# Kernel optimization log

Hardware: AMD Instinct MI355X
Metric: run time of the kernel (lower is better)

## Reference

```python
import jax, jax.numpy as jnp
import numpy as np

N, D_FEAT, HIDDEN, HEADS, NUM_CLASSES = 6000, 512, 256, 8, 32
NEG_INF = -1e9
LEAKY_ALPHA = 0.2


def gat_head(x, adj_bias, W, a1, a2):
    """Single dense GAT attention head (NSL GraphAttnLayer, inference mode).

    x: [N, D], W: [D, F], a1/a2: [F]. Returns [N, F].
    """
    h = x @ W                       # [N, F]
    f1 = h @ a1                     # [N] source term
    f2 = h @ a2                     # [N] destination term
    e = jax.nn.leaky_relu(f1[:, None] + f2[None, :], LEAKY_ALPHA) + adj_bias
    coefs = jax.nn.softmax(e, axis=-1)  # softmax over neighbors j
    return coefs @ h                # [N, F]


def setup_inputs() -> dict:
    key = jax.random.key(0)
    ks = jax.random.split(key, 8)
    features = jax.random.normal(ks[0], (N, D_FEAT), dtype=jnp.float32)
    adj = jax.random.randint(ks[1], (N, N), 0, 2, dtype=jnp.int32)
    # Block 0: 8 heads, each D_FEAT -> HIDDEN
    W0 = jax.random.normal(ks[2], (HEADS, D_FEAT, HIDDEN), dtype=jnp.float32) / np.sqrt(D_FEAT)
    a10 = jax.random.normal(ks[3], (HEADS, HIDDEN), dtype=jnp.float32) / np.sqrt(HIDDEN)
    a20 = jax.random.normal(ks[4], (HEADS, HIDDEN), dtype=jnp.float32) / np.sqrt(HIDDEN)
    # Classifier: single head, HEADS*HIDDEN -> NUM_CLASSES
    Wc = jax.random.normal(ks[5], (HEADS * HIDDEN, NUM_CLASSES), dtype=jnp.float32) / np.sqrt(HEADS * HIDDEN)
    a1c = jax.random.normal(ks[6], (NUM_CLASSES,), dtype=jnp.float32) / np.sqrt(NUM_CLASSES)
    a2c = jax.random.normal(ks[7], (NUM_CLASSES,), dtype=jnp.float32) / np.sqrt(NUM_CLASSES)
    return {"features": features, "adj": adj, "W0": W0, "a10": a10,
            "a20": a20, "Wc": Wc, "a1c": a1c, "a2c": a2c}


def reference(features, adj, W0, a10, a20, Wc, a1c, a2c):
    adj_bias = jnp.where(adj > 0, 0.0, NEG_INF).astype(jnp.float32)  # [N, N]
    # GATBlock: 8 heads concatenated, then ELU (dropout is identity at inference)
    heads = [gat_head(features, adj_bias, W0[h], a10[h], a20[h]) for h in range(HEADS)]
    x = jax.nn.elu(jnp.concatenate(heads, axis=1))  # [N, HEADS*HIDDEN]
    # Classifier GraphAttnLayer -> [N, NUM_CLASSES]
    return gat_head(x, adj_bias, Wc, a1c, a2c)
```

## Files before the change

### kernel.cpp

```cpp
#include <hip/hip_runtime.h>
#include <hip/hip_bf16.h>

#define NN 6000
#define NPAD 6016
#define DF 512
#define HID 256
#define NH 8
#define NC 32
#define FTOT 2048
#define MSTR 96
#define NJB (NPAD / 64)
#define L2E 1.4426950408889634f

using short8 = __attribute__((ext_vector_type(8))) short;
using f32x16 = __attribute__((ext_vector_type(16))) float;
using f32x4  = __attribute__((ext_vector_type(4))) float;

__device__ __forceinline__ unsigned short f2bf(float f) {
    unsigned int u = __float_as_uint(f);
    return (unsigned short)((u + 0x7fffu + ((u >> 16) & 1u)) >> 16);
}
__device__ __forceinline__ float bf2f(unsigned short s) {
    return __uint_as_float(((unsigned int)s) << 16);
}
__device__ __forceinline__ void gl16(const void* g, void* l) {
    __builtin_amdgcn_global_load_lds(
        (const __attribute__((address_space(1))) unsigned int*)g,
        (__attribute__((address_space(3))) unsigned int*)l, 16, 0, 0);
}


__global__ void pack_bits(const int* __restrict__ adj, unsigned char* __restrict__ maskb) {
    int row = blockIdx.y;
    int b = blockIdx.x * 256 + threadIdx.x;
    if (b >= 768) return;
    int j0 = b * 8;
    unsigned int v = 0;
    if (j0 + 7 < NN) {
        const int4* p = (const int4*)(adj + (size_t)row * NN + j0);
        int4 a = p[0], c = p[1];
        v = (unsigned)((a.x>0) | ((a.y>0)<<1) | ((a.z>0)<<2) | ((a.w>0)<<3)
          | ((c.x>0)<<4) | ((c.y>0)<<5) | ((c.z>0)<<6) | ((c.w>0)<<7));
    }
    maskb[(size_t)row * 768 + b] = (unsigned char)v;
}

__global__ void cast_x4(const float* __restrict__ x, unsigned short* __restrict__ xb, int n4) {
    int i = blockIdx.x * 256 + threadIdx.x;
    if (i >= n4) return;
    float4 v = ((const float4*)x)[i];
    unsigned long long pk = (unsigned long long)f2bf(v.x)
        | ((unsigned long long)f2bf(v.y) << 16)
        | ((unsigned long long)f2bf(v.z) << 32)
        | ((unsigned long long)f2bf(v.w) << 48);
    ((unsigned long long*)xb)[i] = pk;
}

__global__ void wt_pack(const float* __restrict__ W0, unsigned short* __restrict__ Wt) {
    int fp = blockIdx.x;
    int h = fp >> 8, f = fp & 255;
    for (int k = threadIdx.x; k < DF; k += 256)
        Wt[(size_t)fp * DF + k] = f2bf(W0[(((size_t)h * DF + k) << 8) | f]);
}

__global__ void wct_pack(const float* __restrict__ Wc, unsigned short* __restrict__ Wct) {
    int c = blockIdx.x;
    for (int k = threadIdx.x; k < FTOT; k += 256)
        Wct[(size_t)c * FTOT + k] = f2bf(Wc[(size_t)k * NC + c]);
}

__global__ __launch_bounds__(256, 2) void gemm_h(const unsigned short* __restrict__ A,
                                                 const unsigned short* __restrict__ B,
                                                 unsigned short* __restrict__ Ht) {
    __shared__ __align__(16) unsigned short As[128 * 64];
    __shared__ __align__(16) unsigned short Bs[128 * 64];
    const int w = threadIdx.x >> 6, l = threadIdx.x & 63;
    const int lrow = l & 31, kh = l >> 5;
    const int wm = w >> 1, wn = w & 1;
    const int mbase = blockIdx.x * 128, nbase = blockIdx.y * 128;
    const int srcc = (l & 7) ^ (l >> 3);
    f32x16 acc[2][2];
#pragma unroll
    for (int i = 0; i < 2; ++i)
#pragma unroll
        for (int j = 0; j < 2; ++j) acc[i][j] = (f32x16)0.0f;

#pragma unroll 1
    for (int kb = 0; kb < DF / 64; ++kb) {
        __syncthreads();
#pragma unroll
        for (int q = 0; q < 4; ++q) {
            int c = q * 4 + w;
            int r = c * 8 + (l >> 3);
            int arow = mbase + r; if (arow > NN - 1) arow = NN - 1;
            gl16(A + (size_t)arow * DF + kb * 64 + srcc * 8, (char*)As + c * 1024);
            gl16(B + (size_t)(nbase + r) * DF + kb * 64 + srcc * 8, (char*)Bs + c * 1024);
        }
        __syncthreads();
#pragma unroll
        for (int kk = 0; kk < 4; ++kk) {
            short8 av[2], bv[2];
#pragma unroll
            for (int mt = 0; mt < 2; ++mt) {
                int r = wm * 64 + mt * 32 + lrow;
                av[mt] = *(const short8*)((const char*)As + r * 128 + ((((kk << 1) | kh) ^ (r & 7)) << 4));
            }
#pragma unroll
            for (int ft = 0; ft < 2; ++ft) {
                int r = wn * 64 + ft * 32 + lrow;
                bv[ft] = *(const short8*)((const char*)Bs + r * 128 + ((((kk << 1) | kh) ^ (r & 7)) << 4));
            }
#pragma unroll
            for (int mt = 0; mt < 2; ++mt)
#pragma unroll
                for (int ft = 0; ft < 2; ++ft)
                    acc[mt][ft] = __builtin_amdgcn_mfma_f32_32x32x16_bf16(av[mt], bv[ft], acc[mt][ft], 0, 0, 0);
        }
    }
#pragma unroll
    for (int mt = 0; mt < 2; ++mt)
#pragma unroll
        for (int ft = 0; ft < 2; ++ft) {
            size_t n = nbase + wn * 64 + ft * 32 + lrow;
#pragma unroll
            for (int g = 0; g < 4; ++g) {
                int m0 = mbase + wm * 64 + mt * 32 + (g << 3) + (kh << 2);
                unsigned long long pk =
                    (unsigned long long)f2bf(acc[mt][ft][g * 4 + 0]) |
                    ((unsigned long long)f2bf(acc[mt][ft][g * 4 + 1]) << 16) |
                    ((unsigned long long)f2bf(acc[mt][ft][g * 4 + 2]) << 32) |
                    ((unsigned long long)f2bf(acc[mt][ft][g * 4 + 3]) << 48);
                *(unsigned long long*)(Ht + n * NPAD + m0) = pk;
            }
        }
}

__global__ void f12_kern(const unsigned short* __restrict__ Ht, const float* __restrict__ a1,
                         const float* __restrict__ a2, float* __restrict__ f1, float* __restrict__ f2,
                         int fdim) {
    int h = blockIdx.y;
    int i = blockIdx.x * 256 + threadIdx.x;
    if (i >= NPAD) return;
    float s1 = 0.f, s2 = 0.f;
    const unsigned short* base = Ht + (size_t)h * fdim * NPAD + i;
    for (int f = 0; f < fdim; ++f) {
        float v = bf2f(base[(size_t)f * NPAD]);
        s1 = fmaf(v, a1[h * fdim + f], s1);
        s2 = fmaf(v, a2[h * fdim + f], s2);
    }
    f1[(size_t)h * NPAD + i] = s1 * L2E;
    f2[(size_t)h * NPAD + i] = s2 * L2E;
}

__global__ void rarb_kern(const float* __restrict__ f1all, const float* __restrict__ f2all,
                          float* __restrict__ RA, float* __restrict__ RB,
                          float* __restrict__ E2F, float* __restrict__ E2Fb) {
    int h = blockIdx.x;
    __shared__ float red[8];
    const float* f2h = f2all + (size_t)h * NPAD;
    float m = -3.0e38f;
    for (int i = threadIdx.x; i < NN; i += 256) m = fmaxf(m, f2h[i]);
    for (int off = 32; off; off >>= 1) m = fmaxf(m, __shfl_xor(m, off));
    if ((threadIdx.x & 63) == 0) red[threadIdx.x >> 6] = m;
    __syncthreads();
    if (threadIdx.x == 0)
        red[4] = fmaxf(fmaxf(red[0], red[1]), fmaxf(red[2], red[3]));
    __syncthreads();
    float Mh = red[4];
    for (int i = threadIdx.x; i < NPAD; i += 256) {
        float F1 = (i < NN) ? f1all[(size_t)h * NPAD + i] : 0.f;
        float t2 = F1 + Mh;
        float Mi = fmaxf(t2, 0.2f * t2);
        RA[(size_t)h * NPAD + i] = F1 - Mi;
        RB[(size_t)h * NPAD + i] = 0.2f * F1 - Mi;
        float v2 = f2h[i];
        E2F[(size_t)h * NPAD + i] = exp2f(v2);
        E2Fb[(size_t)h * NPAD + i] = exp2f(0.2f * v2);
    }
}

__global__ __launch_bounds__(256, 3) void attn_main(
    const unsigned short* __restrict__ Ht,
    const unsigned long long* __restrict__ mask,
    const float* __restrict__ RA, const float* __restrict__ RB,
    const float* __restrict__ E2F, const float* __restrict__ E2Fb,
    unsigned short* __restrict__ x2)
{
    __shared__ __align__(16) unsigned short htile[3 * 128 * 64];
    const int bid = blockIdx.x;
    const int h = bid & 7;
    const int fh = (bid >> 3) & 1;
    const int rowbase = (bid >> 4) * 128;
    const int w = threadIdx.x >> 6, l = threadIdx.x & 63;
    const int lrow = l & 31, kh = l >> 5;
    const int myrow = rowbase + w * 32 + lrow;
    const bool act = myrow < NN;
    const int rowc = act ? myrow : NN - 1;
    const unsigned short* Hh = Ht + ((size_t)h * HID + fh * 128) * NPAD;
    const float* E2Fh = E2F + (size_t)h * NPAD;
    const float* E2Fbh = E2Fb + (size_t)h * NPAD;
    const float era = exp2f(RA[(size_t)h * NPAD + rowc]);
    const float erb = exp2f(RB[(size_t)h * NPAD + rowc]);
    const short8 ones = { (short)0x3F80, (short)0x3F80, (short)0x3F80, (short)0x3F80,
                          (short)0x3F80, (short)0x3F80, (short)0x3F80, (short)0x3F80 };
    f32x16 acc[4];
    f32x16 asum = (f32x16)0.0f;
#pragma unroll
    for (int i = 0; i < 4; ++i) acc[i] = (f32x16)0.0f;

    auto STAGE = [&](int buf, int jb) {
#pragma unroll
        for (int q = 0; q < 4; ++q) {
            int c = q * 4 + w;
            int f = c * 8 + (l >> 3);
            int srcq = (l & 7) ^ (l >> 3) ^ ((c & 1) << 2);
            gl16(Hh + (size_t)f * NPAD + jb * 64 + srcq * 8, (char*)htile + buf * 16384 + c * 1024);
        }
    };

    STAGE(0, 0);
#pragma unroll 1
    for (int jb = 0; jb < NJB; ++jb) {
        if (jb + 1 < NJB) STAGE((jb + 1) % 3, jb + 1);
        asm volatile("s_waitcnt vmcnt(4)" ::: "memory");
        __builtin_amdgcn_sched_barrier(0);
        __builtin_amdgcn_s_barrier();
        __builtin_amdgcn_sched_barrier(0);
        const char* tb = (const char*)htile + (jb % 3) * 16384;
        unsigned long long mw = mask[(size_t)rowc * MSTR + jb];
#pragma unroll
        for (int kk = 0; kk < 4; ++kk) {
            unsigned int mbyte = (unsigned int)((mw >> (kk * 16 + kh * 8)) & 0xffull);
            int j0 = jb * 64 + kk * 16 + kh * 8;
            f32x4 ea0 = *(const f32x4*)(E2Fh + j0);
            f32x4 ea1 = *(const f32x4*)(E2Fh + j0 + 4);
            f32x4 eb0 = *(const f32x4*)(E2Fbh + j0);
            f32x4 eb1 = *(const f32x4*)(E2Fbh + j0 + 4);
            float p[8];
#pragma unroll
            for (int e = 0; e < 8; ++e) {
                float fe = (e < 4) ? ea0[e & 3] : ea1[e & 3];
                float fb = (e < 4) ? eb0[e & 3] : eb1[e & 3];
                float pe = fmaxf(era * fe, erb * fb);
                p[e] = (mbyte & (1u << e)) ? pe : 0.f;
            }
            union { unsigned int u[4]; short8 s8; } cv;
#pragma unroll
            for (int q = 0; q < 4; ++q)
                cv.u[q] = __builtin_amdgcn_perm(__float_as_uint(p[2 * q + 1]),
                                                __float_as_uint(p[2 * q]), 0x07060302u);
            __builtin_amdgcn_s_setprio(1);
            asum = __builtin_amdgcn_mfma_f32_32x32x16_bf16(cv.s8, ones, asum, 0, 0, 0);
#pragma unroll
            for (int ft = 0; ft < 4; ++ft) {
                int fr = ft * 32 + lrow;
                int slot = ((kk * 2 + kh) ^ (fr & 7) ^ (((fr >> 3) & 1) << 2));
                short8 bfrag = *(const short8*)(tb + fr * 128 + (slot << 4));
                acc[ft] = __builtin_amdgcn_mfma_f32_32x32x16_bf16(cv.s8, bfrag, acc[ft], 0, 0, 0);
            }
            __builtin_amdgcn_s_setprio(0);
        }
    }

    float dinv[16];
#pragma unroll
    for (int t = 0; t < 16; ++t)
        dinv[t] = (asum[t] > 0.f) ? (1.0f / asum[t]) : 0.f;

#pragma unroll
    for (int ft = 0; ft < 4; ++ft)
#pragma unroll
        for (int g = 0; g < 4; ++g)
#pragma unroll
            for (int rr = 0; rr < 4; ++rr) {
                int grow = rowbase + w * 32 + (g << 3) + (kh << 2) + rr;
                if (grow < NN) {
                    float v = acc[ft][g * 4 + rr] * dinv[g * 4 + rr];
                    v = (v > 0.f) ? v : (__expf(v) - 1.f);
                    x2[(size_t)grow * FTOT + h * HID + fh * 128 + ft * 32 + lrow] = f2bf(v);
                }
            }
}

__global__ __launch_bounds__(256, 2) void gemm_hc(const unsigned short* __restrict__ A,
                                                  const unsigned short* __restrict__ B,
                                                  float* __restrict__ pk) {
    int w = threadIdx.x >> 6, l = threadIdx.x & 63;
    int lrow = l & 31, kh = l >> 5;
    int q = blockIdx.y;
    int nbase = blockIdx.x * 128 + w * 32;
    int brow = nbase + lrow; if (brow > NN - 1) brow = NN - 1;
    f32x16 acc = (f32x16)0.0f;
    const short8* ap = (const short8*)(A + (size_t)lrow * FTOT + q * 256 + kh * 8);
    const short8* bp = (const short8*)(B + (size_t)brow * FTOT + q * 256 + kh * 8);
#pragma unroll
    for (int kk = 0; kk < 16; ++kk) {
        short8 af = ap[kk * 2];
        short8 bf = bp[kk * 2];
        acc = __builtin_amdgcn_mfma_f32_32x32x16_bf16(af, bf, acc, 0, 0, 0);
    }
    int i = nbase + lrow;
#pragma unroll
    for (int g = 0; g < 4; ++g) {
        int c0 = (g << 3) + (kh << 2);
#pragma unroll
        for (int r = 0; r < 4; ++r)
            pk[((size_t)q * NC + c0 + r) * NPAD + i] = acc[g * 4 + r];
    }
}

__global__ void merge_hc(const float* __restrict__ pk, unsigned short* __restrict__ hct) {
    int i = blockIdx.x * 256 + threadIdx.x;
    int c = blockIdx.y;
    if (i >= NPAD) return;
    float s = 0.f;
#pragma unroll
    for (int q = 0; q < 8; ++q) s += pk[((size_t)q * NC + c) * NPAD + i];
    hct[(size_t)c * NPAD + i] = f2bf(s);
}

__global__ __launch_bounds__(256) void cls_part(
    const unsigned short* __restrict__ hctb,
    const unsigned long long* __restrict__ mask,
    const float* __restrict__ RAc, const float* __restrict__ RBc,
    const float* __restrict__ E2Fc, const float* __restrict__ E2Fcb,
    float* __restrict__ pacc, float* __restrict__ pdsum)
{
    const int w = threadIdx.x >> 6, l = threadIdx.x & 63;
    const int lrow = l & 31, kh = l >> 5;
    const int q = blockIdx.y;
    const int rowbase = blockIdx.x * 128;
    const int myrow = rowbase + w * 32 + lrow;
    const bool act = myrow < NN;
    const float era = exp2f(RAc[myrow]);
    const float erb = exp2f(RBc[myrow]);
    const int JB0 = q * 12, JB1 = (JB0 + 12 < NJB) ? JB0 + 12 : NJB;
    const short8 ones = { (short)0x3F80, (short)0x3F80, (short)0x3F80, (short)0x3F80,
                          (short)0x3F80, (short)0x3F80, (short)0x3F80, (short)0x3F80 };
    f32x16 acc = (f32x16)0.0f;
    f32x16 asum = (f32x16)0.0f;

#pragma unroll 1
    for (int jb = JB0; jb < JB1; ++jb) {
        unsigned long long mword = act ? mask[(size_t)myrow * MSTR + jb] : 0ull;
#pragma unroll
        for (int kk = 0; kk < 4; ++kk) {
            short8 bfrag = *(const short8*)(hctb + (size_t)lrow * NPAD + jb * 64 + (kk * 2 + kh) * 8);
            unsigned int mbyte = (unsigned int)((mword >> (kk * 16 + kh * 8)) & 0xffull);
            int j0 = jb * 64 + kk * 16 + kh * 8;
            f32x4 ea0 = *(const f32x4*)(E2Fc + j0);
            f32x4 ea1 = *(const f32x4*)(E2Fc + j0 + 4);
            f32x4 eb0 = *(const f32x4*)(E2Fcb + j0);
            f32x4 eb1 = *(const f32x4*)(E2Fcb + j0 + 4);
            float p[8];
#pragma unroll
            for (int e = 0; e < 8; ++e) {
                float fe = (e < 4) ? ea0[e & 3] : ea1[e & 3];
                float fb = (e < 4) ? eb0[e & 3] : eb1[e & 3];
                float pe = fmaxf(era * fe, erb * fb);
                p[e] = (mbyte & (1u << e)) ? pe : 0.f;
            }
            union { unsigned int u[4]; short8 s8; } cv;
#pragma unroll
            for (int t = 0; t < 4; ++t)
                cv.u[t] = __builtin_amdgcn_perm(__float_as_uint(p[2 * t + 1]),
                                                __float_as_uint(p[2 * t]), 0x07060302u);
            asum = __builtin_amdgcn_mfma_f32_32x32x16_bf16(cv.s8, ones, asum, 0, 0, 0);
            acc = __builtin_amdgcn_mfma_f32_32x32x16_bf16(cv.s8, bfrag, acc, 0, 0, 0);
        }
    }
#pragma unroll
    for (int g = 0; g < 4; ++g)
#pragma unroll
        for (int rr = 0; rr < 4; ++rr) {
            int i = rowbase + w * 32 + (g << 3) + (kh << 2) + rr;
            pacc[((size_t)q * NPAD + i) * NC + lrow] = acc[g * 4 + rr];
            if (lrow == 0) pdsum[(size_t)q * NPAD + i] = asum[g * 4 + rr];
        }
}

__global__ void cls_merge(const float* __restrict__ pacc, const float* __restrict__ pdsum,
                          float* __restrict__ outp) {
    int i = blockIdx.x * 8 + (threadIdx.x >> 5);
    int c = threadIdx.x & 31;
    if (i >= NN) return;
    float num = 0.f, den = 0.f;
#pragma unroll
    for (int q = 0; q < 8; ++q) {
        num += pacc[((size_t)q * NPAD + i) * NC + c];
        den += pdsum[(size_t)q * NPAD + i];
    }
    outp[(size_t)i * NC + c] = (den > 0.f) ? num / den : 0.f;
}

extern "C" void kernel_launch(void* const* d_in, const int* in_sizes, int n_in,
                              void* d_out, int out_size, void* d_ws, size_t ws_size,
                              hipStream_t stream) {
    const float* features = (const float*)d_in[0];
    const int*   adj      = (const int*)d_in[1];
    const float* W0       = (const float*)d_in[2];
    const float* a10      = (const float*)d_in[3];
    const float* a20      = (const float*)d_in[4];
    const float* Wc       = (const float*)d_in[5];
    const float* a1c      = (const float*)d_in[6];
    const float* a2c      = (const float*)d_in[7];
    float* out = (float*)d_out;

    char* p = (char*)d_ws;
    auto alloc = [&](size_t bytes) { char* r = p; p += (bytes + 255) & ~(size_t)255; return r; };
    unsigned long long* mask = (unsigned long long*)alloc((size_t)NN * MSTR * 8);
    unsigned short* Xbf = (unsigned short*)alloc((size_t)NN * DF * 2);
    unsigned short* Wt  = (unsigned short*)alloc((size_t)FTOT * DF * 2);
    unsigned short* Ht  = (unsigned short*)alloc((size_t)FTOT * NPAD * 2);
    unsigned short* x2  = (unsigned short*)alloc((size_t)NN * FTOT * 2);
    unsigned short* Wct = (unsigned short*)alloc((size_t)NC * FTOT * 2);
    unsigned short* hct = (unsigned short*)alloc((size_t)NC * NPAD * 2);
    float* f1  = (float*)alloc((size_t)NH * NPAD * 4);
    float* f2  = (float*)alloc((size_t)NH * NPAD * 4);
    float* RA  = (float*)alloc((size_t)NH * NPAD * 4);
    float* RB  = (float*)alloc((size_t)NH * NPAD * 4);
    float* E2F  = (float*)alloc((size_t)NH * NPAD * 4);
    float* E2Fb = (float*)alloc((size_t)NH * NPAD * 4);
    float* f1c  = (float*)alloc((size_t)NPAD * 4);
    float* f2c  = (float*)alloc((size_t)NPAD * 4);
    float* RAc  = (float*)alloc((size_t)NPAD * 4);
    float* RBc  = (float*)alloc((size_t)NPAD * 4);
    float* E2Fc  = (float*)alloc((size_t)NPAD * 4);
    float* E2Fcb = (float*)alloc((size_t)NPAD * 4);
    float* pkhc  = (float*)Xbf;
    float* pacc  = (float*)Xbf;
    float* pdsum = pacc + (size_t)8 * NPAD * NC;

    pack_bits<<<dim3(3, NN), 256, 0, stream>>>(adj, (unsigned char*)mask);
    cast_x4<<<(NN * DF / 4 + 255) / 256, 256, 0, stream>>>(features, Xbf, NN * DF / 4);
    wt_pack<<<FTOT, 256, 0, stream>>>(W0, Wt);
    wct_pack<<<NC, 256, 0, stream>>>(Wc, Wct);

    gemm_h<<<dim3(NPAD / 128, FTOT / 128), 256, 0, stream>>>(Xbf, Wt, Ht);
    f12_kern<<<dim3((NPAD + 255) / 256, NH), 256, 0, stream>>>(Ht, a10, a20, f1, f2, HID);
    rarb_kern<<<NH, 256, 0, stream>>>(f1, f2, RA, RB, E2F, E2Fb);

    attn_main<<<dim3(47 * 2 * NH), 256, 0, stream>>>(Ht, mask, RA, RB, E2F, E2Fb, x2);

    gemm_hc<<<dim3(NPAD / 128, 8), 256, 0, stream>>>(Wct, x2, pkhc);
    merge_hc<<<dim3((NPAD + 255) / 256, NC), 256, 0, stream>>>(pkhc, hct);
    f12_kern<<<dim3((NPAD + 255) / 256, 1), 256, 0, stream>>>(hct, a1c, a2c, f1c, f2c, NC);
    rarb_kern<<<1, 256, 0, stream>>>(f1c, f2c, RAc, RBc, E2Fc, E2Fcb);

    cls_part<<<dim3(47, 8), 256, 0, stream>>>(hct, mask, RAc, RBc, E2Fc, E2Fcb, pacc, pdsum);
    cls_merge<<<750, 256, 0, stream>>>(pacc, pdsum, out);
}
```

Before: 448.7 us.

## Switch attention kernel to 16x16x32 MFMA with full-head feature tiles

The attention kernel now uses 16x16x32 bf16 MFMAs, with each block covering 64 rows and all 256 features of a head instead of 128 rows and half the features. The probability matrix is therefore computed once per row per head rather than twice (once per feature half), which removes duplicated exp/mask work and mask loads. The H tile is staged as 32-column slabs with a new swizzle. In exchange each thread holds 16 f32x4 accumulators, the MFMA shape is smaller, and each staged H tile is reused by fewer rows.

```diff
diff --git a/kernel.cpp b/kernel.cpp
--- a/kernel.cpp
+++ b/kernel.cpp
@@ -10,6 +10,7 @@
 #define FTOT 2048
 #define MSTR 96
 #define NJB (NPAD / 64)
+#define NJT (NPAD / 32)
 #define L2E 1.4426950408889634f
 
 using short8 = __attribute__((ext_vector_type(8))) short;
@@ -186,100 +187,95 @@
     const float* __restrict__ E2F, const float* __restrict__ E2Fb,
     unsigned short* __restrict__ x2)
 {
-    __shared__ __align__(16) unsigned short htile[3 * 128 * 64];
+    __shared__ __align__(16) unsigned short htile[3 * 256 * 32];
     const int bid = blockIdx.x;
     const int h = bid & 7;
-    const int fh = (bid >> 3) & 1;
-    const int rowbase = (bid >> 4) * 128;
+    const int rowbase = (bid >> 3) * 64;
     const int w = threadIdx.x >> 6, l = threadIdx.x & 63;
-    const int lrow = l & 31, kh = l >> 5;
-    const int myrow = rowbase + w * 32 + lrow;
-    const bool act = myrow < NN;
-    const int rowc = act ? myrow : NN - 1;
-    const unsigned short* Hh = Ht + ((size_t)h * HID + fh * 128) * NPAD;
+    const int la = l & 15;
+    const int s  = l >> 4;
+    const int rowA = rowbase + w * 16 + la;
+    const int rowAc = (rowA < NN) ? rowA : NN - 1;
+    const unsigned short* Hh = Ht + (size_t)h * HID * NPAD;
     const float* E2Fh = E2F + (size_t)h * NPAD;
     const float* E2Fbh = E2Fb + (size_t)h * NPAD;
-    const float era = exp2f(RA[(size_t)h * NPAD + rowc]);
-    const float erb = exp2f(RB[(size_t)h * NPAD + rowc]);
+    const float era = exp2f(RA[(size_t)h * NPAD + rowAc]);
+    const float erb = exp2f(RB[(size_t)h * NPAD + rowAc]);
     const short8 ones = { (short)0x3F80, (short)0x3F80, (short)0x3F80, (short)0x3F80,
                           (short)0x3F80, (short)0x3F80, (short)0x3F80, (short)0x3F80 };
-    f32x16 acc[4];
-    f32x16 asum = (f32x16)0.0f;
-#pragma unroll
-    for (int i = 0; i < 4; ++i) acc[i] = (f32x16)0.0f;
-
-    auto STAGE = [&](int buf, int jb) {
+    f32x4 acc16[16];
+    f32x4 asum4 = (f32x4)0.0f;
+#pragma unroll
+    for (int i = 0; i < 16; ++i) acc16[i] = (f32x4)0.0f;
+
+    const int segsrc = (l & 3) ^ ((l >> 2) & 3);
+    auto STAGE = [&](int buf, int jt) {
 #pragma unroll
         for (int q = 0; q < 4; ++q) {
             int c = q * 4 + w;
-            int f = c * 8 + (l >> 3);
-            int srcq = (l & 7) ^ (l >> 3) ^ ((c & 1) << 2);
-            gl16(Hh + (size_t)f * NPAD + jb * 64 + srcq * 8, (char*)htile + buf * 16384 + c * 1024);
+            int f = c * 16 + (l >> 2);
+            gl16(Hh + (size_t)f * NPAD + jt * 32 + segsrc * 8,
+                 (char*)htile + buf * 16384 + c * 1024);
         }
     };
 
     STAGE(0, 0);
 #pragma unroll 1
-    for (int jb = 0; jb < NJB; ++jb) {
-        if (jb + 1 < NJB) STAGE((jb + 1) % 3, jb + 1);
+    for (int jt = 0; jt < NJT; ++jt) {
+        if (jt + 1 < NJT) STAGE((jt + 1) % 3, jt + 1);
         asm volatile("s_waitcnt vmcnt(4)" ::: "memory");
         __builtin_amdgcn_sched_barrier(0);
         __builtin_amdgcn_s_barrier();
         __builtin_amdgcn_sched_barrier(0);
-        const char* tb = (const char*)htile + (jb % 3) * 16384;
-        unsigned long long mw = mask[(size_t)rowc * MSTR + jb];
-#pragma unroll
-        for (int kk = 0; kk < 4; ++kk) {
-            unsigned int mbyte = (unsigned int)((mw >> (kk * 16 + kh * 8)) & 0xffull);
-            int j0 = jb * 64 + kk * 16 + kh * 8;
-            f32x4 ea0 = *(const f32x4*)(E2Fh + j0);
-            f32x4 ea1 = *(const f32x4*)(E2Fh + j0 + 4);
-            f32x4 eb0 = *(const f32x4*)(E2Fbh + j0);
-            f32x4 eb1 = *(const f32x4*)(E2Fbh + j0 + 4);
-            float p[8];
-#pragma unroll
-            for (int e = 0; e < 8; ++e) {
-                float fe = (e < 4) ? ea0[e & 3] : ea1[e & 3];
-                float fb = (e < 4) ? eb0[e & 3] : eb1[e & 3];
-                float pe = fmaxf(era * fe, erb * fb);
-                p[e] = (mbyte & (1u << e)) ? pe : 0.f;
+        const char* tb = (const char*)htile + (jt % 3) * 16384;
+        unsigned int mwrd = ((const unsigned int*)mask)[(size_t)rowAc * 192 + jt];
+        unsigned int mbyte = (mwrd >> (s * 8)) & 0xffu;
+        int j0 = jt * 32 + s * 8;
+        f32x4 ea0 = *(const f32x4*)(E2Fh + j0);
+        f32x4 ea1 = *(const f32x4*)(E2Fh + j0 + 4);
+        f32x4 eb0 = *(const f32x4*)(E2Fbh + j0);
+        f32x4 eb1 = *(const f32x4*)(E2Fbh + j0 + 4);
+        float p[8];
+#pragma unroll
+        for (int e = 0; e < 8; ++e) {
+            float fe = (e < 4) ? ea0[e & 3] : ea1[e & 3];
+            float fb = (e < 4) ? eb0[e & 3] : eb1[e & 3];
+            float pe = fmaxf(era * fe, erb * fb);
+            p[e] = (mbyte & (1u << e)) ? pe : 0.f;
+        }
+        union { unsigned int u[4]; short8 s8; } cv;
+#pragma unroll
+        for (int q = 0; q < 4; ++q)
+            cv.u[q] = __builtin_amdgcn_perm(__float_as_uint(p[2 * q + 1]),
+                                            __float_as_uint(p[2 * q]), 0x07060302u);
+        __builtin_amdgcn_s_setprio(1);
+        asum4 = __builtin_amdgcn_mfma_f32_16x16x32_bf16(cv.s8, ones, asum4, 0, 0, 0);
+#pragma unroll
+        for (int ft = 0; ft < 16; ++ft) {
+            int fl = ft * 16 + la;
+            int slot = s ^ (fl & 3);
+            short8 bfrag = *(const short8*)(tb + fl * 64 + slot * 16);
+            acc16[ft] = __builtin_amdgcn_mfma_f32_16x16x32_bf16(cv.s8, bfrag, acc16[ft], 0, 0, 0);
+        }
+        __builtin_amdgcn_s_setprio(0);
+    }
+
+    float dinv[4];
+#pragma unroll
+    for (int t = 0; t < 4; ++t)
+        dinv[t] = (asum4[t] > 0.f) ? (1.0f / asum4[t]) : 0.f;
+
+#pragma unroll
+    for (int ft = 0; ft < 16; ++ft)
+#pragma unroll
+        for (int t = 0; t < 4; ++t) {
+            int grow = rowbase + w * 16 + s * 4 + t;
+            if (grow < NN) {
+                float v = acc16[ft][t] * dinv[t];
+                v = (v > 0.f) ? v : (__expf(v) - 1.f);
+                x2[(size_t)grow * FTOT + h * HID + ft * 16 + la] = f2bf(v);
             }
-            union { unsigned int u[4]; short8 s8; } cv;
-#pragma unroll
-            for (int q = 0; q < 4; ++q)
-                cv.u[q] = __builtin_amdgcn_perm(__float_as_uint(p[2 * q + 1]),
-                                                __float_as_uint(p[2 * q]), 0x07060302u);
-            __builtin_amdgcn_s_setprio(1);
-            asum = __builtin_amdgcn_mfma_f32_32x32x16_bf16(cv.s8, ones, asum, 0, 0, 0);
-#pragma unroll
-            for (int ft = 0; ft < 4; ++ft) {
-                int fr = ft * 32 + lrow;
-                int slot = ((kk * 2 + kh) ^ (fr & 7) ^ (((fr >> 3) & 1) << 2));
-                short8 bfrag = *(const short8*)(tb + fr * 128 + (slot << 4));
-                acc[ft] = __builtin_amdgcn_mfma_f32_32x32x16_bf16(cv.s8, bfrag, acc[ft], 0, 0, 0);
-            }
-            __builtin_amdgcn_s_setprio(0);
-        }
-    }
-
-    float dinv[16];
-#pragma unroll
-    for (int t = 0; t < 16; ++t)
-        dinv[t] = (asum[t] > 0.f) ? (1.0f / asum[t]) : 0.f;
-
-#pragma unroll
-    for (int ft = 0; ft < 4; ++ft)
-#pragma unroll
-        for (int g = 0; g < 4; ++g)
-#pragma unroll
-            for (int rr = 0; rr < 4; ++rr) {
-                int grow = rowbase + w * 32 + (g << 3) + (kh << 2) + rr;
-                if (grow < NN) {
-                    float v = acc[ft][g * 4 + rr] * dinv[g * 4 + rr];
-                    v = (v > 0.f) ? v : (__expf(v) - 1.f);
-                    x2[(size_t)grow * FTOT + h * HID + fh * 128 + ft * 32 + lrow] = f2bf(v);
-                }
-            }
+        }
 }
 
 __global__ __launch_bounds__(256, 2) void gemm_hc(const unsigned short* __restrict__ A,
@@ -440,7 +436,7 @@
     f12_kern<<<dim3((NPAD + 255) / 256, NH), 256, 0, stream>>>(Ht, a10, a20, f1, f2, HID);
     rarb_kern<<<NH, 256, 0, stream>>>(f1, f2, RA, RB, E2F, E2Fb);
 
-    attn_main<<<dim3(47 * 2 * NH), 256, 0, stream>>>(Ht, mask, RA, RB, E2F, E2Fb, x2);
+    attn_main<<<dim3(94 * NH), 256, 0, stream>>>(Ht, mask, RA, RB, E2F, E2Fb, x2);
 
     gemm_hc<<<dim3(NPAD / 128, 8), 256, 0, stream>>>(Wct, x2, pkhc);
     merge_hc<<<dim3((NPAD + 255) / 256, NC), 256, 0, stream>>>(pkhc, hct);
```

Result: faster. 427.4 us (-4.8%).
